# Kernel optimization log

Hardware: AMD Instinct MI355X
Metric: run time of the kernel (lower is better)

## Reference

```python
import jax, jax.numpy as jnp
import numpy as np

CENTER_VAR = 0.1
SIZE_VAR = 0.2
EPS = 1e-8


def setup_inputs() -> dict:
    key = jax.random.key(0)
    k1, k2, k3, k4, k5, k6 = jax.random.split(key, 6)
    B, P, C = 8, 2048, 21
    confidence = jax.random.normal(k1, (B, P, C), dtype=jnp.float32)
    locations = jax.random.normal(k2, (B, P, 4), dtype=jnp.float32)
    target_confidence = jax.random.randint(k3, (B, P), 0, 2).astype(jnp.int64)
    target_locations = jax.random.normal(k4, (B, P, 4), dtype=jnp.float32)
    # priors in center-offset form (cx, cy, w, h), valid positive sizes
    cxcy = jax.random.uniform(k5, (P, 2), jnp.float32, 0.05, 0.95)
    wh = jax.random.uniform(k6, (P, 2), jnp.float32, 0.02, 0.3)
    priors = jnp.concatenate([cxcy, wh], axis=-1)
    return {"confidence": confidence, "locations": locations,
            "target_confidence": target_confidence,
            "target_locations": target_locations, "priors": priors}


def _decode(loc, priors):
    # loc: [B,P,4], priors: [P,4] center form -> corner-form boxes [B,P,4]
    cxcy = priors[None, :, 0:2] + loc[:, :, 0:2] * CENTER_VAR * priors[None, :, 2:4]
    wh = priors[None, :, 2:4] * jnp.exp(loc[:, :, 2:4] * SIZE_VAR)
    mn = cxcy - wh * 0.5
    return jnp.concatenate([mn, mn + wh], axis=-1)


def _giou_pair(a, b):
    # a: [A,4], b: [B,4] corner form -> pairwise GIoU [A,B]
    inter_mx = jnp.minimum(a[:, None, 2:4], b[None, :, 2:4])
    inter_mn = jnp.maximum(a[:, None, 0:2], b[None, :, 0:2])
    inter = jnp.prod(jnp.clip(inter_mx - inter_mn, 0.0, None), axis=-1)
    area_a = ((a[:, 2] - a[:, 0]) * (a[:, 3] - a[:, 1]))[:, None]
    area_b = ((b[:, 2] - b[:, 0]) * (b[:, 3] - b[:, 1]))[None, :]
    union = area_a + area_b - inter
    iou = inter / jnp.maximum(union, EPS)
    enc_mx = jnp.maximum(a[:, None, 2:4], b[None, :, 2:4])
    enc_mn = jnp.minimum(a[:, None, 0:2], b[None, :, 0:2])
    enc = jnp.prod(enc_mx - enc_mn, axis=-1)
    return iou - (enc - union) / jnp.maximum(enc, EPS)


def reference(confidence, locations, target_confidence, target_locations, priors):
    probs = jax.nn.softmax(confidence, axis=-1)
    max_p = probs.max(axis=-1)
    max_i = probs.argmax(axis=-1)
    pos_target = target_confidence > 0                       # [B,P]
    pos_infer = pos_target & (max_p > 0.5) & (max_i > 0)     # [B,P]
    dec_loc = _decode(locations, priors)                     # [B,P,4]
    dec_tgt = _decode(target_locations, priors)              # [B,P,4]

    def per_batch(dl, dt, mi, mt):
        g = _giou_pair(dl, dt)                               # [P,P]
        pair_mask = mi[:, None] & mt[None, :]
        s = jnp.sum(jnp.where(pair_mask, g, 0.0))
        nt = jnp.sum(mt).astype(jnp.float32)
        na = jnp.sum(mi).astype(jnp.float32)
        both = (nt > 0) & (na > 0)
        one = (nt > 0) ^ (na > 0)
        # sum_b[pos_t] (1 - sum_a[pos_i] giou[a,b] / nt) = nt - s/nt
        term = jnp.where(both, nt - s / jnp.maximum(nt, 1.0),
                         jnp.where(one, 1.0, 0.0))
        return term, nt

    terms, nts = jax.vmap(per_batch)(dec_loc, dec_tgt, pos_infer, pos_target)
    num_boxes = jnp.sum(nts)
    return jnp.sum(terms) / jnp.maximum(num_boxes, 1.0)
```

## Files before the change

### kernel.cpp

```cpp
#include <hip/hip_runtime.h>

#define EPSV 1e-8f
#define CENTER_VAR 0.1f
#define SIZE_VAR 0.2f
#define MAXP 2048
#define BLK 1024

__device__ __forceinline__ float4 decode_box(float4 loc, float4 pr) {
    float cx = pr.x + loc.x * CENTER_VAR * pr.z;
    float cy = pr.y + loc.y * CENTER_VAR * pr.w;
    float w  = pr.z * __expf(loc.z * SIZE_VAR);
    float h  = pr.w * __expf(loc.w * SIZE_VAR);
    float x0 = cx - w * 0.5f;
    float y0 = cy - h * 0.5f;
    return make_float4(x0, y0, x0 + w, y0 + h);
}

__device__ __forceinline__ float giou_pair(float4 A, float4 Bx) {
    float ix = fminf(A.z, Bx.z) - fmaxf(A.x, Bx.x);
    float iy = fminf(A.w, Bx.w) - fmaxf(A.y, Bx.y);
    float inter = fmaxf(ix, 0.f) * fmaxf(iy, 0.f);
    float area_a = (A.z - A.x) * (A.w - A.y);
    float area_b = (Bx.z - Bx.x) * (Bx.w - Bx.y);
    float uni = area_a + area_b - inter;
    float iou = __fdividef(inter, fmaxf(uni, EPSV));
    float ex = fmaxf(A.z, Bx.z) - fminf(A.x, Bx.x);
    float ey = fmaxf(A.w, Bx.w) - fminf(A.y, Bx.y);
    float enc = ex * ey;
    return iou - __fdividef(enc - uni, fmaxf(enc, EPSV));
}

__global__ __launch_bounds__(BLK) void fused_kernel(
    const float* __restrict__ conf,
    const float* __restrict__ loc,
    const int*   __restrict__ tconf,
    const float* __restrict__ tloc,
    const float* __restrict__ priors,
    int P, int C,
    float* __restrict__ term_out, float* __restrict__ nt_out) {
    int b = blockIdx.x;
    __shared__ float4 ab[MAXP];
    __shared__ int nA_sh;
    __shared__ float red_f[BLK / 64];
    __shared__ int   red_i[BLK / 64];
    if (threadIdx.x == 0) nA_sh = 0;
    __syncthreads();

    const size_t base = (size_t)b * P;

    for (int p = threadIdx.x; p < P; p += BLK) {
        size_t idx = base + p;
        if (tconf[idx] > 0) {
            const float* cf = conf + idx * C;
            float m; int mi; float se;
            if (C == 21) {
                float v[21];
                #pragma unroll
                for (int c = 0; c < 21; ++c) v[c] = cf[c];
                m = v[0]; mi = 0;
                #pragma unroll
                for (int c = 1; c < 21; ++c) { if (v[c] > m) { m = v[c]; mi = c; } }
                se = 0.f;
                #pragma unroll
                for (int c = 0; c < 21; ++c) se += __expf(v[c] - m);
            } else {
                m = cf[0]; mi = 0;
                for (int c = 1; c < C; ++c) { float v = cf[c]; if (v > m) { m = v; mi = c; } }
                se = 0.f;
                for (int c = 0; c < C; ++c) se += __expf(cf[c] - m);
            }
            if (se < 2.0f && mi > 0) {
                float4 l  = ((const float4*)loc)[idx];
                float4 pr = ((const float4*)priors)[p];
                int k = atomicAdd(&nA_sh, 1);
                if (k < MAXP) ab[k] = decode_box(l, pr);
            }
        }
    }
    __syncthreads();
    int nA = nA_sh;

    float acc = 0.f;
    int   ntc = 0;
    for (int p = threadIdx.x; p < P; p += BLK) {
        size_t idx = base + p;
        if (tconf[idx] > 0) {
            ++ntc;
            float4 l  = ((const float4*)tloc)[idx];
            float4 pr = ((const float4*)priors)[p];
            float4 T = decode_box(l, pr);
            for (int i = 0; i < nA; ++i) acc += giou_pair(ab[i], T);
        }
    }

    int lane = threadIdx.x & 63, wid = threadIdx.x >> 6;
    for (int off = 32; off > 0; off >>= 1) {
        acc += __shfl_down(acc, off);
        ntc += __shfl_down(ntc, off);
    }
    if (lane == 0) { red_f[wid] = acc; red_i[wid] = ntc; }
    __syncthreads();
    if (threadIdx.x == 0) {
        float s = 0.f; int nt = 0;
        for (int w = 0; w < BLK / 64; ++w) { s += red_f[w]; nt += red_i[w]; }
        float ntf = (float)nt;
        bool bt = nt > 0, ba = nA > 0;
        float term = (bt && ba) ? (ntf - s / fmaxf(ntf, 1.f))
                                : ((bt != ba) ? 1.f : 0.f);
        term_out[b] = term;
        nt_out[b]   = ntf;
    }
}

__global__ void finalize_kernel(const float* __restrict__ term,
                                const float* __restrict__ ntf,
                                int B, float* __restrict__ out) {
    if (threadIdx.x != 0 || blockIdx.x != 0) return;
    float tsum = 0.f, nsum = 0.f;
    for (int b = 0; b < B; ++b) { tsum += term[b]; nsum += ntf[b]; }
    out[0] = tsum / fmaxf(nsum, 1.f);
}

extern "C" void kernel_launch(void* const* d_in, const int* in_sizes, int n_in,
                              void* d_out, int out_size, void* d_ws, size_t ws_size,
                              hipStream_t stream) {
    const float* conf   = (const float*)d_in[0];
    const float* loc    = (const float*)d_in[1];
    const int*   tconf  = (const int*)  d_in[2];
    const float* tloc   = (const float*)d_in[3];
    const float* priors = (const float*)d_in[4];
    float* out = (float*)d_out;

    int P = in_sizes[4] / 4;
    int B = in_sizes[2] / P;
    int C = in_sizes[0] / (B * P);

    float* term = (float*)d_ws;
    float* ntf  = term + 64;

    fused_kernel<<<B, BLK, 0, stream>>>(conf, loc, tconf, tloc, priors,
                                        P, C, term, ntf);
    finalize_kernel<<<1, 64, 0, stream>>>(term, ntf, B, out);
}
```

Measured before the change: 73.94 us.

## Split each batch across many blocks with a cooperative grid-synced kernel

Replaces the one-block-per-batch kernel (8 blocks of 1024 threads) with a cooperative launch of B*ceil(P/256) blocks of 256 threads. Each block filters and decodes its slice of predicted boxes into a global scratch region. After a grid sync, every block gathers its batch's full list of predicted boxes into shared memory and computes GIoU sums for its own targets. A second grid sync lets block 0 do the final reduction, which removes the separate finalize launch. The aim is to use far more compute units for the O(P^2) pair work, at the cost of two grid-wide barriers and some global scratch traffic.

Result: slower. 106.5 us (+44.0%).

```diff
diff --git a/kernel.cpp b/kernel.cpp
--- a/kernel.cpp
+++ b/kernel.cpp
@@ -1,10 +1,13 @@
 #include <hip/hip_runtime.h>
+#include <hip/hip_cooperative_groups.h>
+
+namespace cg = cooperative_groups;
 
 #define EPSV 1e-8f
 #define CENTER_VAR 0.1f
 #define SIZE_VAR 0.2f
-#define MAXP 2048
-#define BLK 1024
+#define TPB 256
+#define MAXA 2048
 
 __device__ __forceinline__ float4 decode_box(float4 loc, float4 pr) {
     float cx = pr.x + loc.x * CENTER_VAR * pr.z;
@@ -30,95 +33,132 @@
     return iou - __fdividef(enc - uni, fmaxf(enc, EPSV));
 }
 
-__global__ __launch_bounds__(BLK) void fused_kernel(
+__global__ __launch_bounds__(TPB) void fused_coop(
     const float* __restrict__ conf,
     const float* __restrict__ loc,
     const int*   __restrict__ tconf,
     const float* __restrict__ tloc,
     const float* __restrict__ priors,
-    int P, int C,
-    float* __restrict__ term_out, float* __restrict__ nt_out) {
-    int b = blockIdx.x;
-    __shared__ float4 ab[MAXP];
-    __shared__ int nA_sh;
-    __shared__ float red_f[BLK / 64];
-    __shared__ int   red_i[BLK / 64];
-    if (threadIdx.x == 0) nA_sh = 0;
+    int B, int P, int C, int bpb,
+    int*    __restrict__ cnt_a,
+    int*    __restrict__ cnt_t,
+    float*  __restrict__ s_part,
+    float4* __restrict__ regions,
+    float*  __restrict__ out) {
+    cg::grid_group grid = cg::this_grid();
+
+    int blk = blockIdx.x;
+    int b   = blk / bpb;
+    int sub = blk - b * bpb;
+    int p   = sub * TPB + threadIdx.x;
+    size_t idx = (size_t)b * P + p;
+    bool live = p < P;
+    int lane = threadIdx.x & 63, wid = threadIdx.x >> 6;
+
+    __shared__ int   na_sh;
+    __shared__ int   wcnt[TPB / 64];
+    __shared__ float wsum[TPB / 64];
+    __shared__ float4 ab[MAXA];
+
+    if (threadIdx.x == 0) na_sh = 0;
     __syncthreads();
 
-    const size_t base = (size_t)b * P;
+    bool pos_t = live && (tconf[idx] > 0);
+    unsigned long long bm = __ballot(pos_t);
+    if (lane == 0) wcnt[wid] = __popcll(bm);
 
-    for (int p = threadIdx.x; p < P; p += BLK) {
-        size_t idx = base + p;
-        if (tconf[idx] > 0) {
-            const float* cf = conf + idx * C;
-            float m; int mi; float se;
-            if (C == 21) {
-                float v[21];
-                #pragma unroll
-                for (int c = 0; c < 21; ++c) v[c] = cf[c];
-                m = v[0]; mi = 0;
-                #pragma unroll
-                for (int c = 1; c < 21; ++c) { if (v[c] > m) { m = v[c]; mi = c; } }
-                se = 0.f;
-                #pragma unroll
-                for (int c = 0; c < 21; ++c) se += __expf(v[c] - m);
-            } else {
-                m = cf[0]; mi = 0;
-                for (int c = 1; c < C; ++c) { float v = cf[c]; if (v > m) { m = v; mi = c; } }
-                se = 0.f;
-                for (int c = 0; c < C; ++c) se += __expf(cf[c] - m);
-            }
-            if (se < 2.0f && mi > 0) {
-                float4 l  = ((const float4*)loc)[idx];
-                float4 pr = ((const float4*)priors)[p];
-                int k = atomicAdd(&nA_sh, 1);
-                if (k < MAXP) ab[k] = decode_box(l, pr);
-            }
+    if (pos_t) {
+        const float* cf = conf + idx * C;
+        float m; int mi; float se;
+        if (C == 21) {
+            float v[21];
+            #pragma unroll
+            for (int c = 0; c < 21; ++c) v[c] = cf[c];
+            m = v[0]; mi = 0;
+            #pragma unroll
+            for (int c = 1; c < 21; ++c) { if (v[c] > m) { m = v[c]; mi = c; } }
+            se = 0.f;
+            #pragma unroll
+            for (int c = 0; c < 21; ++c) se += __expf(v[c] - m);
+        } else {
+            m = cf[0]; mi = 0;
+            for (int c = 1; c < C; ++c) { float v = cf[c]; if (v > m) { m = v; mi = c; } }
+            se = 0.f;
+            for (int c = 0; c < C; ++c) se += __expf(cf[c] - m);
+        }
+        if (se < 2.0f && mi > 0) {
+            float4 l  = ((const float4*)loc)[idx];
+            float4 pr = ((const float4*)priors)[p];
+            int k = atomicAdd(&na_sh, 1);
+            regions[(size_t)blk * TPB + k] = decode_box(l, pr);
         }
     }
     __syncthreads();
-    int nA = nA_sh;
+    if (threadIdx.x == 0) {
+        int c = 0;
+        #pragma unroll
+        for (int w = 0; w < TPB / 64; ++w) c += wcnt[w];
+        cnt_t[blk] = c;
+        cnt_a[blk] = na_sh;
+    }
+
+    grid.sync();
+
+    int nA = 0;
+    for (int r = 0; r < bpb; ++r) {
+        int c = cnt_a[b * bpb + r];
+        int take = min(c, MAXA - nA);
+        for (int i = threadIdx.x; i < take; i += TPB)
+            ab[nA + i] = regions[(size_t)(b * bpb + r) * TPB + i];
+        nA += take;
+    }
+    __syncthreads();
 
     float acc = 0.f;
-    int   ntc = 0;
-    for (int p = threadIdx.x; p < P; p += BLK) {
-        size_t idx = base + p;
-        if (tconf[idx] > 0) {
-            ++ntc;
-            float4 l  = ((const float4*)tloc)[idx];
-            float4 pr = ((const float4*)priors)[p];
-            float4 T = decode_box(l, pr);
-            for (int i = 0; i < nA; ++i) acc += giou_pair(ab[i], T);
+    if (pos_t && nA > 0) {
+        float4 l  = ((const float4*)tloc)[idx];
+        float4 pr = ((const float4*)priors)[p];
+        float4 T = decode_box(l, pr);
+        for (int i = 0; i < nA; ++i) acc += giou_pair(ab[i], T);
+    }
+    for (int off = 32; off > 0; off >>= 1) acc += __shfl_down(acc, off);
+    if (lane == 0) wsum[wid] = acc;
+    __syncthreads();
+    if (threadIdx.x == 0) {
+        float t = 0.f;
+        #pragma unroll
+        for (int w = 0; w < TPB / 64; ++w) t += wsum[w];
+        s_part[blk] = t;
+    }
+
+    grid.sync();
+
+    if (blk == 0) {
+        __shared__ float tterm[TPB];
+        __shared__ float tnt[TPB];
+        float term = 0.f, ntf = 0.f;
+        if (threadIdx.x < B) {
+            int bb = threadIdx.x;
+            int nt = 0, na = 0; float s = 0.f;
+            for (int r = 0; r < bpb; ++r) {
+                nt += cnt_t[bb * bpb + r];
+                na += cnt_a[bb * bpb + r];
+                s  += s_part[bb * bpb + r];
+            }
+            ntf = (float)nt;
+            bool bt = nt > 0, ba = na > 0;
+            term = (bt && ba) ? (ntf - s / fmaxf(ntf, 1.f))
+                              : ((bt != ba) ? 1.f : 0.f);
+        }
+        tterm[threadIdx.x] = term;
+        tnt[threadIdx.x]   = ntf;
+        __syncthreads();
+        if (threadIdx.x == 0) {
+            float tsum = 0.f, nsum = 0.f;
+            for (int bb = 0; bb < B; ++bb) { tsum += tterm[bb]; nsum += tnt[bb]; }
+            out[0] = tsum / fmaxf(nsum, 1.f);
         }
     }
-
-    int lane = threadIdx.x & 63, wid = threadIdx.x >> 6;
-    for (int off = 32; off > 0; off >>= 1) {
-        acc += __shfl_down(acc, off);
-        ntc += __shfl_down(ntc, off);
-    }
-    if (lane == 0) { red_f[wid] = acc; red_i[wid] = ntc; }
-    __syncthreads();
-    if (threadIdx.x == 0) {
-        float s = 0.f; int nt = 0;
-        for (int w = 0; w < BLK / 64; ++w) { s += red_f[w]; nt += red_i[w]; }
-        float ntf = (float)nt;
-        bool bt = nt > 0, ba = nA > 0;
-        float term = (bt && ba) ? (ntf - s / fmaxf(ntf, 1.f))
-                                : ((bt != ba) ? 1.f : 0.f);
-        term_out[b] = term;
-        nt_out[b]   = ntf;
-    }
-}
-
-__global__ void finalize_kernel(const float* __restrict__ term,
-                                const float* __restrict__ ntf,
-                                int B, float* __restrict__ out) {
-    if (threadIdx.x != 0 || blockIdx.x != 0) return;
-    float tsum = 0.f, nsum = 0.f;
-    for (int b = 0; b < B; ++b) { tsum += term[b]; nsum += ntf[b]; }
-    out[0] = tsum / fmaxf(nsum, 1.f);
 }
 
 extern "C" void kernel_launch(void* const* d_in, const int* in_sizes, int n_in,
@@ -134,11 +174,19 @@
     int P = in_sizes[4] / 4;
     int B = in_sizes[2] / P;
     int C = in_sizes[0] / (B * P);
+    int bpb  = (P + TPB - 1) / TPB;
+    int nblk = B * bpb;
 
-    float* term = (float*)d_ws;
-    float* ntf  = term + 64;
+    int*   cnt_a  = (int*)d_ws;
+    int*   cnt_t  = cnt_a + nblk;
+    float* s_part = (float*)(cnt_t + nblk);
+    size_t hdr = ((size_t)nblk * 3 * sizeof(int) + 15) & ~(size_t)15;
+    float4* regions = (float4*)((char*)d_ws + hdr);
 
-    fused_kernel<<<B, BLK, 0, stream>>>(conf, loc, tconf, tloc, priors,
-                                        P, C, term, ntf);
-    finalize_kernel<<<1, 64, 0, stream>>>(term, ntf, B, out);
+    void* args[] = { (void*)&conf, (void*)&loc, (void*)&tconf, (void*)&tloc,
+                     (void*)&priors, (void*)&B, (void*)&P, (void*)&C, (void*)&bpb,
+                     (void*)&cnt_a, (void*)&cnt_t, (void*)&s_part,
+                     (void*)&regions, (void*)&out };
+    hipLaunchCooperativeKernel((void*)fused_coop, dim3(nblk), dim3(TPB),
+                               args, 0, stream);
 }
```

## Split per-batch GIoU into many wave-sized blocks with ballot compaction and last-block finalize

Applied to the files above, without the earlier changes.

The old version ran one 1024-thread block per batch element, which used only 8 workgroups on the GPU. The work is now split into two kernels launched over B*(P/64) single-wavefront blocks. The mask kernel computes the softmax-based inference mask and compacts decoded boxes per wave with ballot/popcount, with no shared atomics. The pair kernel gathers each batch's compacted boxes into LDS, accumulates GIoU sums per target, and a last-block-done atomic performs the final reduction, which removes the separate finalize kernel. In exchange, every block of a batch rebuilds the same box list in LDS, and the workspace now needs room for the per-block regions.

After: 83.82 us. +13.4%, slower.

```diff
diff --git a/kernel.cpp b/kernel.cpp
--- a/kernel.cpp
+++ b/kernel.cpp
@@ -3,8 +3,8 @@
 #define EPSV 1e-8f
 #define CENTER_VAR 0.1f
 #define SIZE_VAR 0.2f
-#define MAXP 2048
-#define BLK 1024
+#define WSZ 64
+#define MAXA 2048
 
 __device__ __forceinline__ float4 decode_box(float4 loc, float4 pr) {
     float cx = pr.x + loc.x * CENTER_VAR * pr.z;
@@ -30,95 +30,144 @@
     return iou - __fdividef(enc - uni, fmaxf(enc, EPSV));
 }
 
-__global__ __launch_bounds__(BLK) void fused_kernel(
+__global__ __launch_bounds__(WSZ) void mask_kernel(
     const float* __restrict__ conf,
     const float* __restrict__ loc,
     const int*   __restrict__ tconf,
+    const float* __restrict__ priors,
+    int P, int C, int bpb,
+    int* __restrict__ done,
+    int* __restrict__ cnt_a, int* __restrict__ cnt_t,
+    float4* __restrict__ regions) {
+    int blk = blockIdx.x;
+    int lane = threadIdx.x;
+    int b = blk / bpb;
+    int p = (blk - b * bpb) * WSZ + lane;
+    size_t idx = (size_t)b * P + p;
+    bool live = p < P;
+
+    if (blk == 0 && lane == 0) *done = 0;
+
+    bool pos_t = live && (tconf[idx] > 0);
+    unsigned long long bm_t = __ballot(pos_t);
+
+    bool inf = false;
+    float4 box = make_float4(0.f, 0.f, 0.f, 0.f);
+    if (pos_t) {
+        const float* cf = conf + idx * C;
+        float m; int mi; float se;
+        if (C == 21) {
+            float v[21];
+            #pragma unroll
+            for (int c = 0; c < 21; ++c) v[c] = cf[c];
+            m = v[0]; mi = 0;
+            #pragma unroll
+            for (int c = 1; c < 21; ++c) { if (v[c] > m) { m = v[c]; mi = c; } }
+            se = 0.f;
+            #pragma unroll
+            for (int c = 0; c < 21; ++c) se += __expf(v[c] - m);
+        } else {
+            m = cf[0]; mi = 0;
+            for (int c = 1; c < C; ++c) { float v = cf[c]; if (v > m) { m = v; mi = c; } }
+            se = 0.f;
+            for (int c = 0; c < C; ++c) se += __expf(cf[c] - m);
+        }
+        if (se < 2.0f && mi > 0) {
+            float4 l  = ((const float4*)loc)[idx];
+            float4 pr = ((const float4*)priors)[p];
+            box = decode_box(l, pr);
+            inf = true;
+        }
+    }
+    unsigned long long bm_i = __ballot(inf);
+    if (inf) {
+        int k = __popcll(bm_i & ((1ull << lane) - 1ull));
+        regions[(size_t)blk * WSZ + k] = box;
+    }
+    if (lane == 0) {
+        cnt_t[blk] = __popcll(bm_t);
+        cnt_a[blk] = __popcll(bm_i);
+    }
+}
+
+__global__ __launch_bounds__(WSZ) void pair_kernel(
+    const int*   __restrict__ tconf,
     const float* __restrict__ tloc,
     const float* __restrict__ priors,
-    int P, int C,
-    float* __restrict__ term_out, float* __restrict__ nt_out) {
-    int b = blockIdx.x;
-    __shared__ float4 ab[MAXP];
-    __shared__ int nA_sh;
-    __shared__ float red_f[BLK / 64];
-    __shared__ int   red_i[BLK / 64];
-    if (threadIdx.x == 0) nA_sh = 0;
-    __syncthreads();
-
-    const size_t base = (size_t)b * P;
-
-    for (int p = threadIdx.x; p < P; p += BLK) {
-        size_t idx = base + p;
-        if (tconf[idx] > 0) {
-            const float* cf = conf + idx * C;
-            float m; int mi; float se;
-            if (C == 21) {
-                float v[21];
-                #pragma unroll
-                for (int c = 0; c < 21; ++c) v[c] = cf[c];
-                m = v[0]; mi = 0;
-                #pragma unroll
-                for (int c = 1; c < 21; ++c) { if (v[c] > m) { m = v[c]; mi = c; } }
-                se = 0.f;
-                #pragma unroll
-                for (int c = 0; c < 21; ++c) se += __expf(v[c] - m);
-            } else {
-                m = cf[0]; mi = 0;
-                for (int c = 1; c < C; ++c) { float v = cf[c]; if (v > m) { m = v; mi = c; } }
-                se = 0.f;
-                for (int c = 0; c < C; ++c) se += __expf(cf[c] - m);
-            }
-            if (se < 2.0f && mi > 0) {
-                float4 l  = ((const float4*)loc)[idx];
-                float4 pr = ((const float4*)priors)[p];
-                int k = atomicAdd(&nA_sh, 1);
-                if (k < MAXP) ab[k] = decode_box(l, pr);
-            }
+    const float4* __restrict__ regions,
+    const int* __restrict__ cnt_a, const int* __restrict__ cnt_t,
+    int* __restrict__ done,
+    float* __restrict__ s_part,
+    int B, int P, int bpb, int nblk,
+    float* __restrict__ out) {
+    int blk = blockIdx.x;
+    int lane = threadIdx.x;
+    int b = blk / bpb;
+    int base = b * bpb;
+    int p = (blk - base) * WSZ + lane;
+    size_t idx = (size_t)b * P + p;
+    bool live = p < P;
+
+    __shared__ float4 ab[MAXA];
+    __shared__ int cnts[64];
+
+    cnts[lane] = (lane < bpb) ? cnt_a[base + lane] : 0;
+    __syncthreads();
+    int nA = 0;
+    for (int r = 0; r < bpb; ++r) {
+        int c = cnts[r];
+        for (int i = lane; i < c; i += WSZ)
+            ab[nA + i] = regions[(size_t)(base + r) * WSZ + i];
+        nA += c;
+    }
+    __syncthreads();
+
+    bool pos_t = live && (tconf[idx] > 0);
+    float acc = 0.f;
+    if (pos_t && nA > 0) {
+        float4 l  = ((const float4*)tloc)[idx];
+        float4 pr = ((const float4*)priors)[p];
+        float4 T = decode_box(l, pr);
+        for (int i = 0; i < nA; ++i) acc += giou_pair(ab[i], T);
+    }
+    for (int off = 32; off > 0; off >>= 1) acc += __shfl_down(acc, off);
+    if (lane == 0) s_part[blk] = acc;
+    __threadfence();
+
+    int last = 0;
+    if (lane == 0) {
+        int old = __hip_atomic_fetch_add(done, 1, __ATOMIC_ACQ_REL,
+                                         __HIP_MEMORY_SCOPE_AGENT);
+        last = (old == nblk - 1);
+    }
+    last = __shfl(last, 0);
+    if (!last) return;
+
+    __shared__ float sb[16];
+    __shared__ int   ntb[16], nab[16];
+    if (lane < 16) { sb[lane] = 0.f; ntb[lane] = 0; nab[lane] = 0; }
+    __syncthreads();
+    for (int slot = lane; slot < nblk; slot += WSZ) {
+        int bb = slot / bpb;
+        float sv = __hip_atomic_load(&s_part[slot], __ATOMIC_RELAXED,
+                                     __HIP_MEMORY_SCOPE_AGENT);
+        atomicAdd(&sb[bb], sv);
+        atomicAdd(&ntb[bb], cnt_t[slot]);
+        atomicAdd(&nab[bb], cnt_a[slot]);
+    }
+    __syncthreads();
+    if (lane == 0) {
+        float tsum = 0.f, nsum = 0.f;
+        for (int bb = 0; bb < B; ++bb) {
+            float ntf = (float)ntb[bb];
+            bool bt = ntb[bb] > 0, ba = nab[bb] > 0;
+            float term = (bt && ba) ? (ntf - sb[bb] / fmaxf(ntf, 1.f))
+                                    : ((bt != ba) ? 1.f : 0.f);
+            tsum += term;
+            nsum += ntf;
         }
-    }
-    __syncthreads();
-    int nA = nA_sh;
-
-    float acc = 0.f;
-    int   ntc = 0;
-    for (int p = threadIdx.x; p < P; p += BLK) {
-        size_t idx = base + p;
-        if (tconf[idx] > 0) {
-            ++ntc;
-            float4 l  = ((const float4*)tloc)[idx];
-            float4 pr = ((const float4*)priors)[p];
-            float4 T = decode_box(l, pr);
-            for (int i = 0; i < nA; ++i) acc += giou_pair(ab[i], T);
-        }
-    }
-
-    int lane = threadIdx.x & 63, wid = threadIdx.x >> 6;
-    for (int off = 32; off > 0; off >>= 1) {
-        acc += __shfl_down(acc, off);
-        ntc += __shfl_down(ntc, off);
-    }
-    if (lane == 0) { red_f[wid] = acc; red_i[wid] = ntc; }
-    __syncthreads();
-    if (threadIdx.x == 0) {
-        float s = 0.f; int nt = 0;
-        for (int w = 0; w < BLK / 64; ++w) { s += red_f[w]; nt += red_i[w]; }
-        float ntf = (float)nt;
-        bool bt = nt > 0, ba = nA > 0;
-        float term = (bt && ba) ? (ntf - s / fmaxf(ntf, 1.f))
-                                : ((bt != ba) ? 1.f : 0.f);
-        term_out[b] = term;
-        nt_out[b]   = ntf;
-    }
-}
-
-__global__ void finalize_kernel(const float* __restrict__ term,
-                                const float* __restrict__ ntf,
-                                int B, float* __restrict__ out) {
-    if (threadIdx.x != 0 || blockIdx.x != 0) return;
-    float tsum = 0.f, nsum = 0.f;
-    for (int b = 0; b < B; ++b) { tsum += term[b]; nsum += ntf[b]; }
-    out[0] = tsum / fmaxf(nsum, 1.f);
+        out[0] = tsum / fmaxf(nsum, 1.f);
+    }
 }
 
 extern "C" void kernel_launch(void* const* d_in, const int* in_sizes, int n_in,
@@ -134,11 +183,19 @@
     int P = in_sizes[4] / 4;
     int B = in_sizes[2] / P;
     int C = in_sizes[0] / (B * P);
-
-    float* term = (float*)d_ws;
-    float* ntf  = term + 64;
-
-    fused_kernel<<<B, BLK, 0, stream>>>(conf, loc, tconf, tloc, priors,
-                                        P, C, term, ntf);
-    finalize_kernel<<<1, 64, 0, stream>>>(term, ntf, B, out);
-}
+    int bpb  = (P + WSZ - 1) / WSZ;
+    int nblk = B * bpb;
+
+    int*   done   = (int*)d_ws;
+    int*   cnt_a  = done + 4;
+    int*   cnt_t  = cnt_a + nblk;
+    float* s_part = (float*)(cnt_t + nblk);
+    size_t hdr = (16 + (size_t)nblk * 3 * sizeof(int) + 15) & ~(size_t)15;
+    float4* regions = (float4*)((char*)d_ws + hdr);
+
+    mask_kernel<<<nblk, WSZ, 0, stream>>>(conf, loc, tconf, priors,
+                                          P, C, bpb, done, cnt_a, cnt_t, regions);
+    pair_kernel<<<nblk, WSZ, 0, stream>>>(tconf, tloc, priors, regions,
+                                          cnt_a, cnt_t, done, s_part,
+                                          B, P, bpb, nblk, out);
+}
```
